# Performance work log

Hardware: AMD Instinct MI355X
Metric: run time of the kernel (lower is better)

The kernel has to match this reference:

```python
import jax, jax.numpy as jnp
import numpy as np

C_MID = 32  # inChannels // 8
# Packing order matches torch loop: diagonal offset -i for i in 0..C-1,
# i.e. pairs (j+i, j) for j in 0..C-1-i, concatenated.
_ROWS = np.concatenate([np.arange(C_MID - i) + i for i in range(C_MID)])
_COLS = np.concatenate([np.arange(C_MID - i) for i in range(C_MID)])


def _bn_relu(y, g, b, m, v, eps=1e-5):
    # y: (B, C, H, W); per-channel affine BN (eval-style) + relu
    inv = g / jnp.sqrt(v + eps)
    return jax.nn.relu(y * inv[:, None, None] + (b - m * inv)[:, None, None])


def setup_inputs() -> dict:
    key = jax.random.key(0)
    ks = jax.random.split(key, 14)
    B, Cin, H, W = 16, 256, 64, 64
    mid, T, Cout = C_MID, C_MID * (C_MID + 1) // 2, 256
    return {
        "x": jax.random.normal(ks[0], (B, Cin, H, W), jnp.float32),
        "w1": jax.random.normal(ks[1], (mid, Cin), jnp.float32) * 0.05,
        "b1": jax.random.normal(ks[2], (mid,), jnp.float32) * 0.05,
        "g1": jax.random.uniform(ks[3], (mid,), jnp.float32, 0.5, 1.5),
        "be1": jax.random.normal(ks[4], (mid,), jnp.float32) * 0.1,
        "m1": jax.random.normal(ks[5], (mid,), jnp.float32) * 0.1,
        "v1": jax.random.uniform(ks[6], (mid,), jnp.float32, 0.5, 1.5),
        "w2": jax.random.normal(ks[7], (Cout, T), jnp.float32) * 0.05,
        "b2": jax.random.normal(ks[8], (Cout,), jnp.float32) * 0.05,
        "g2": jax.random.uniform(ks[9], (Cout,), jnp.float32, 0.5, 1.5),
        "be2": jax.random.normal(ks[10], (Cout,), jnp.float32) * 0.1,
        "m2": jax.random.normal(ks[11], (Cout,), jnp.float32) * 0.1,
        "v2": jax.random.uniform(ks[12], (Cout,), jnp.float32, 0.5, 1.5),
    }


def reference(x, w1, b1, g1, be1, m1, v1, w2, b2, g2, be2, m2, v2):
    # dimReduceLayer1: 1x1 conv + BN + relu
    y = jnp.einsum('bchw,oc->bohw', x, w1) + b1[:, None, None]
    y = _bn_relu(y, g1, be1, m1, v1)                       # (B, mid, H, W)
    yb = jnp.transpose(y, (0, 2, 3, 1))                    # (B, H, W, mid)
    rows = jnp.asarray(_ROWS)
    cols = jnp.asarray(_COLS)
    # Packed lower-triangular bilinear features, exactly the torch diagonal+cat order.
    packed = yb[..., rows] * yb[..., cols]                 # (B, H, W, T)
    # dimReduceLayer2: 1x1 conv + BN + relu
    z = jnp.einsum('bhwt,ot->bohw', packed, w2) + b2[:, None, None]
    return _bn_relu(z, g2, be2, m2, v2)
```

## Files before the change

kernel.cpp:

```cpp
#include <hip/hip_runtime.h>

#define EPS 1e-5f

typedef float f32x4 __attribute__((ext_vector_type(4)));
typedef short bf16x8 __attribute__((ext_vector_type(8)));

__device__ __forceinline__ unsigned short f2bf(float f) {
  unsigned int u = __builtin_bit_cast(unsigned int, f);
  u = (u + 0x7FFFu + ((u >> 16) & 1u)) >> 16;
  return (unsigned short)u;
}

__global__ __launch_bounds__(256) void k_prep(
    const float* __restrict__ w1, const float* __restrict__ b1,
    const float* __restrict__ g1, const float* __restrict__ be1,
    const float* __restrict__ m1, const float* __restrict__ v1,
    const float* __restrict__ w2, const float* __restrict__ b2,
    const float* __restrict__ g2, const float* __restrict__ be2,
    const float* __restrict__ m2, const float* __restrict__ v2,
    float* __restrict__ beta1, float* __restrict__ beta2,
    unsigned short* __restrict__ w1b, unsigned short* __restrict__ w2f)
{
  int t = blockIdx.x * 256 + threadIdx.x;
  if (t < 139264) {
    int j = t & 7, l = (t >> 3) & 63, g = t >> 9;
    int ct = g & 15, ks = g >> 4;
    int k = ks * 32 + (l >> 4) * 8 + j;
    int ch = ct * 16 + (l & 15);
    float val = 0.f;
    if (k < 528) {
      float s2 = g2[ch] * rsqrtf(v2[ch] + EPS);
      val = w2[ch * 528 + k] * s2;
    }
    w2f[t] = f2bf(val);
  }
  if (t < 8192) {
    int j = t & 7, l = (t >> 3) & 63, g = t >> 9;
    int ct = g & 1, ks = g >> 1;
    int c = ks * 32 + (l >> 4) * 8 + j;
    int m = ct * 16 + (l & 15);
    float s1 = g1[m] * rsqrtf(v1[m] + EPS);
    w1b[t] = f2bf(w1[m * 256 + c] * s1);
  }
  if (t < 32) {
    float s1 = g1[t] * rsqrtf(v1[t] + EPS);
    beta1[t] = (b1[t] - m1[t]) * s1 + be1[t];
  }
  if (t < 256) {
    float s2 = g2[t] * rsqrtf(v2[t] + EPS);
    beta2[t] = (b2[t] - m2[t]) * s2 + be2[t];
  }
}

template<int I>
__device__ __forceinline__ void do_diag(const float* __restrict__ y,
                                        unsigned short* __restrict__ pr)
{
  constexpr int L = 32 - I;
  constexpr int base = 32 * I - (I * (I - 1)) / 2;
  float p[L];
#pragma unroll
  for (int j = 0; j < L; ++j) p[j] = y[I + j] * y[j];
  constexpr int s = (base & 1) ? 1 : 0;
  if constexpr (s != 0) pr[base] = f2bf(p[0]);
#pragma unroll
  for (int j = s; j + 1 < L; j += 2)
    *(unsigned int*)&pr[base + j] =
        (unsigned int)f2bf(p[j]) | ((unsigned int)f2bf(p[j + 1]) << 16);
  if constexpr (((L - s) & 1) != 0) pr[base + L - 1] = f2bf(p[L - 1]);
}

template<int S>
__device__ __forceinline__ void do_set(const float* __restrict__ y,
                                       unsigned short* __restrict__ pr)
{
  do_diag<S>(y, pr);
  do_diag<31 - S>(y, pr);
  do_diag<S + 8>(y, pr);
  do_diag<23 - S>(y, pr);
}

__global__ __launch_bounds__(256, 4) void k_fused(
    const float* __restrict__ x, const unsigned short* __restrict__ w1b,
    const float* __restrict__ beta1, const unsigned short* __restrict__ w2f,
    const float* __restrict__ beta2, float* __restrict__ out)
{
  __shared__ __align__(16) unsigned short pk[32 * 548];
  __shared__ __align__(8) float yf[32 * 34];
  int tid = threadIdx.x;
  int wv = tid >> 6, lane = tid & 63;
  int l15 = lane & 15, l4 = lane >> 4;
  int g = blockIdx.x;
  int orig = ((g & 7) << 8) + (g >> 3);
  int pb = orig * 32;
  int b = pb >> 12, hw0 = pb & 4095;
  const float* xb = x + ((size_t)b << 20) + hw0;

  unsigned short* xt = pk;
  {
    int q = tid & 7;
    int cg = tid >> 3;
#pragma unroll
    for (int pass = 0; pass < 2; ++pass) {
      int c4 = cg + pass * 32;
      float4 v[4];
#pragma unroll
      for (int i = 0; i < 4; ++i)
        v[i] = *(const float4*)&xb[(size_t)(4 * c4 + i) * 4096 + 4 * q];
#pragma unroll
      for (int s = 0; s < 4; ++s) {
        float e0 = ((const float*)&v[0])[s];
        float e1 = ((const float*)&v[1])[s];
        float e2 = ((const float*)&v[2])[s];
        float e3 = ((const float*)&v[3])[s];
        unsigned int lo = (unsigned int)f2bf(e0) | ((unsigned int)f2bf(e1) << 16);
        unsigned int hi = (unsigned int)f2bf(e2) | ((unsigned int)f2bf(e3) << 16);
        *(uint2*)&xt[(4 * q + s) * 276 + 4 * c4] = make_uint2(lo, hi);
      }
    }
  }
  __syncthreads();

  {
    int pxt = wv & 1, mt = wv >> 1;
    int px = pxt * 16 + l15;
    f32x4 acc1 = (f32x4){0.f, 0.f, 0.f, 0.f};
    const uint4* w1b4 = (const uint4*)w1b;
#pragma unroll
    for (int ks = 0; ks < 8; ++ks) {
      union { uint4 q; bf16x8 v; } A, B;
      A.q = w1b4[(ks * 2 + mt) * 64 + lane];
      const unsigned short* s = &xt[px * 276 + ks * 32 + l4 * 8];
      uint2 lo = *(const uint2*)s;
      uint2 hi = *(const uint2*)(s + 4);
      B.q = make_uint4(lo.x, lo.y, hi.x, hi.y);
      acc1 = __builtin_amdgcn_mfma_f32_16x16x32_bf16(A.v, B.v, acc1, 0, 0, 0);
    }
    int m0 = mt * 16 + l4 * 4;
#pragma unroll
    for (int r = 0; r < 4; ++r)
      yf[px * 34 + m0 + r] = fmaxf(acc1[r] + beta1[m0 + r], 0.f);
  }
  __syncthreads();

  {
    int px2 = tid & 31, set = tid >> 5;
    const float* yr = &yf[px2 * 34];
    unsigned short* pr = &pk[px2 * 548];
    float y[32];
#pragma unroll
    for (int k = 0; k < 16; ++k) {
      float2 v = *(const float2*)&yr[2 * k];
      y[2 * k] = v.x; y[2 * k + 1] = v.y;
    }
    switch (set) {
      case 0: do_set<0>(y, pr); break;
      case 1: do_set<1>(y, pr); break;
      case 2: do_set<2>(y, pr); break;
      case 3: do_set<3>(y, pr); break;
      case 4: do_set<4>(y, pr); break;
      case 5: do_set<5>(y, pr); break;
      case 6: do_set<6>(y, pr); break;
      default: do_set<7>(y, pr); break;
    }
    if (set < 4) {
      *(unsigned int*)&pr[528 + set * 4] = 0u;
      *(unsigned int*)&pr[530 + set * 4] = 0u;
    }
  }

  float bet[4][4];
#pragma unroll
  for (int ctl = 0; ctl < 4; ++ctl)
#pragma unroll
    for (int r = 0; r < 4; ++r)
      bet[ctl][r] = beta2[(wv * 4 + ctl) * 16 + l4 * 4 + r];

  __syncthreads();

  f32x4 acc[2][4];
#pragma unroll
  for (int a = 0; a < 2; ++a)
#pragma unroll
    for (int c = 0; c < 4; ++c)
      acc[a][c] = (f32x4){0.f, 0.f, 0.f, 0.f};

  const uint4* w2f4 = (const uint4*)w2f;
#pragma unroll
  for (int ks = 0; ks < 17; ++ks) {
    union { uint4 q; bf16x8 v; } A[4], B[2];
#pragma unroll
    for (int ctl = 0; ctl < 4; ++ctl)
      A[ctl].q = w2f4[(ks * 16 + wv * 4 + ctl) * 64 + lane];
#pragma unroll
    for (int pt = 0; pt < 2; ++pt) {
      const unsigned short* src = &pk[(pt * 16 + l15) * 548 + ks * 32 + l4 * 8];
      uint2 lo = *(const uint2*)src;
      uint2 hi = *(const uint2*)(src + 4);
      B[pt].q = make_uint4(lo.x, lo.y, hi.x, hi.y);
    }
#pragma unroll
    for (int pt = 0; pt < 2; ++pt)
#pragma unroll
      for (int ctl = 0; ctl < 4; ++ctl)
        acc[pt][ctl] = __builtin_amdgcn_mfma_f32_16x16x32_bf16(
            A[ctl].v, B[pt].v, acc[pt][ctl], 0, 0, 0);
  }

#pragma unroll
  for (int pt = 0; pt < 2; ++pt) {
    int hw = hw0 + pt * 16 + l15;
#pragma unroll
    for (int ctl = 0; ctl < 4; ++ctl) {
      int ch = (wv * 4 + ctl) * 16 + l4 * 4;
#pragma unroll
      for (int r = 0; r < 4; ++r) {
        float v = fmaxf(acc[pt][ctl][r] + bet[ctl][r], 0.f);
        out[(((size_t)b * 256 + (ch + r)) << 12) + hw] = v;
      }
    }
  }
}

extern "C" void kernel_launch(void* const* d_in, const int* in_sizes, int n_in,
                              void* d_out, int out_size, void* d_ws, size_t ws_size,
                              hipStream_t stream)
{
  const float* x   = (const float*)d_in[0];
  const float* w1  = (const float*)d_in[1];
  const float* b1  = (const float*)d_in[2];
  const float* g1  = (const float*)d_in[3];
  const float* be1 = (const float*)d_in[4];
  const float* m1  = (const float*)d_in[5];
  const float* v1  = (const float*)d_in[6];
  const float* w2  = (const float*)d_in[7];
  const float* b2  = (const float*)d_in[8];
  const float* g2  = (const float*)d_in[9];
  const float* be2 = (const float*)d_in[10];
  const float* m2  = (const float*)d_in[11];
  const float* v2  = (const float*)d_in[12];

  char* ws = (char*)d_ws;
  float*          beta1 = (float*)(ws);
  float*          beta2 = (float*)(ws + 128);
  unsigned short* w1b   = (unsigned short*)(ws + 1152);
  unsigned short* w2f   = (unsigned short*)(ws + 17536);
  float* out = (float*)d_out;

  k_prep<<<dim3(544), dim3(256), 0, stream>>>(
      w1, b1, g1, be1, m1, v1, w2, b2, g2, be2, m2, v2, beta1, beta2, w1b, w2f);
  k_fused<<<dim3(2048), dim3(256), 0, stream>>>(x, w1b, beta1, w2f, beta2, out);
}
```

Measured before the change: 48.60 us.

## Split fused kernel into layer1 and layer2 kernels with larger pixel tiles

The single fused kernel becomes two kernels. The first computes the 1x1 conv with BN and ReLU and writes bf16 activations to a workspace. The second expands the bilinear features for 128 pixels per block of 512 threads and runs the second GEMM, so each weight fragment load is reused across more pixel tiles. The float-to-bf16 conversion also switches to the packed hardware instruction. This adds a global round trip for the intermediate activations, an extra launch, and a large shared buffer (about 140KB) that limits the second kernel to one block per CU.

```diff
diff --git a/kernel.cpp b/kernel.cpp
--- a/kernel.cpp
+++ b/kernel.cpp
@@ -9,6 +9,15 @@
   unsigned int u = __builtin_bit_cast(unsigned int, f);
   u = (u + 0x7FFFu + ((u >> 16) & 1u)) >> 16;
   return (unsigned short)u;
+}
+__device__ __forceinline__ float bf2f(unsigned short h) {
+  unsigned int u = ((unsigned int)h) << 16;
+  return __builtin_bit_cast(float, u);
+}
+__device__ __forceinline__ unsigned int cvt2(float a, float b) {
+  unsigned int r;
+  asm("v_cvt_pk_bf16_f32 %0, %1, %2" : "=v"(r) : "v"(a), "v"(b));
+  return r;
 }
 
 __global__ __launch_bounds__(256) void k_prep(
@@ -52,41 +61,11 @@
   }
 }
 
-template<int I>
-__device__ __forceinline__ void do_diag(const float* __restrict__ y,
-                                        unsigned short* __restrict__ pr)
-{
-  constexpr int L = 32 - I;
-  constexpr int base = 32 * I - (I * (I - 1)) / 2;
-  float p[L];
-#pragma unroll
-  for (int j = 0; j < L; ++j) p[j] = y[I + j] * y[j];
-  constexpr int s = (base & 1) ? 1 : 0;
-  if constexpr (s != 0) pr[base] = f2bf(p[0]);
-#pragma unroll
-  for (int j = s; j + 1 < L; j += 2)
-    *(unsigned int*)&pr[base + j] =
-        (unsigned int)f2bf(p[j]) | ((unsigned int)f2bf(p[j + 1]) << 16);
-  if constexpr (((L - s) & 1) != 0) pr[base + L - 1] = f2bf(p[L - 1]);
-}
-
-template<int S>
-__device__ __forceinline__ void do_set(const float* __restrict__ y,
-                                       unsigned short* __restrict__ pr)
-{
-  do_diag<S>(y, pr);
-  do_diag<31 - S>(y, pr);
-  do_diag<S + 8>(y, pr);
-  do_diag<23 - S>(y, pr);
-}
-
-__global__ __launch_bounds__(256, 4) void k_fused(
+__global__ __launch_bounds__(256) void k_l1(
     const float* __restrict__ x, const unsigned short* __restrict__ w1b,
-    const float* __restrict__ beta1, const unsigned short* __restrict__ w2f,
-    const float* __restrict__ beta2, float* __restrict__ out)
-{
-  __shared__ __align__(16) unsigned short pk[32 * 548];
-  __shared__ __align__(8) float yf[32 * 34];
+    const float* __restrict__ beta1, unsigned short* __restrict__ yws)
+{
+  __shared__ __align__(16) unsigned short xt[32 * 276];
   int tid = threadIdx.x;
   int wv = tid >> 6, lane = tid & 63;
   int l15 = lane & 15, l4 = lane >> 4;
@@ -96,7 +75,6 @@
   int b = pb >> 12, hw0 = pb & 4095;
   const float* xb = x + ((size_t)b << 20) + hw0;
 
-  unsigned short* xt = pk;
   {
     int q = tid & 7;
     int cg = tid >> 3;
@@ -109,13 +87,12 @@
         v[i] = *(const float4*)&xb[(size_t)(4 * c4 + i) * 4096 + 4 * q];
 #pragma unroll
       for (int s = 0; s < 4; ++s) {
-        float e0 = ((const float*)&v[0])[s];
-        float e1 = ((const float*)&v[1])[s];
-        float e2 = ((const float*)&v[2])[s];
-        float e3 = ((const float*)&v[3])[s];
-        unsigned int lo = (unsigned int)f2bf(e0) | ((unsigned int)f2bf(e1) << 16);
-        unsigned int hi = (unsigned int)f2bf(e2) | ((unsigned int)f2bf(e3) << 16);
-        *(uint2*)&xt[(4 * q + s) * 276 + 4 * c4] = make_uint2(lo, hi);
+        const float* e0 = (const float*)&v[0];
+        const float* e1 = (const float*)&v[1];
+        const float* e2 = (const float*)&v[2];
+        const float* e3 = (const float*)&v[3];
+        *(uint2*)&xt[(4 * q + s) * 276 + 4 * c4] =
+            make_uint2(cvt2(e0[s], e1[s]), cvt2(e2[s], e3[s]));
       }
     }
   }
@@ -137,85 +114,144 @@
       acc1 = __builtin_amdgcn_mfma_f32_16x16x32_bf16(A.v, B.v, acc1, 0, 0, 0);
     }
     int m0 = mt * 16 + l4 * 4;
+    float v0 = fmaxf(acc1[0] + beta1[m0 + 0], 0.f);
+    float v1 = fmaxf(acc1[1] + beta1[m0 + 1], 0.f);
+    float v2 = fmaxf(acc1[2] + beta1[m0 + 2], 0.f);
+    float v3 = fmaxf(acc1[3] + beta1[m0 + 3], 0.f);
+    *(uint2*)&yws[(size_t)(pb + px) * 32 + m0] =
+        make_uint2(cvt2(v0, v1), cvt2(v2, v3));
+  }
+}
+
+template<int I>
+__device__ __forceinline__ void do_diag(const float* __restrict__ y,
+                                        unsigned short* __restrict__ pr)
+{
+  constexpr int L = 32 - I;
+  constexpr int base = 32 * I - (I * (I - 1)) / 2;
+  float p[L];
+#pragma unroll
+  for (int j = 0; j < L; ++j) p[j] = y[I + j] * y[j];
+  constexpr int s = (base & 1) ? 1 : 0;
+  if constexpr (s != 0) pr[base] = f2bf(p[0]);
+#pragma unroll
+  for (int j = s; j + 1 < L; j += 2)
+    *(unsigned int*)&pr[base + j] = cvt2(p[j], p[j + 1]);
+  if constexpr (((L - s) & 1) != 0) pr[base + L - 1] = f2bf(p[L - 1]);
+}
+
+template<int S>
+__device__ __forceinline__ void do_set(const float* __restrict__ y,
+                                       unsigned short* __restrict__ pr)
+{
+  do_diag<S>(y, pr);
+  do_diag<31 - S>(y, pr);
+  do_diag<S + 8>(y, pr);
+  do_diag<23 - S>(y, pr);
+}
+
+__device__ __forceinline__ void p2_slice(const unsigned short* __restrict__ yws,
+                                         int pb, int px_base,
+                                         unsigned short* __restrict__ pk,
+                                         int tid256)
+{
+  int px2 = tid256 & 31, set = tid256 >> 5;
+  int pxl = px_base + px2;
+  const uint4* y4 = (const uint4*)(yws + (size_t)(pb + pxl) * 32);
+  float y[32];
+#pragma unroll
+  for (int qq = 0; qq < 4; ++qq) {
+    uint4 v = y4[qq];
+    unsigned int ua[4] = {v.x, v.y, v.z, v.w};
+#pragma unroll
+    for (int w = 0; w < 4; ++w) {
+      y[qq * 8 + 2 * w]     = bf2f((unsigned short)(ua[w] & 0xFFFFu));
+      y[qq * 8 + 2 * w + 1] = bf2f((unsigned short)(ua[w] >> 16));
+    }
+  }
+  unsigned short* pr = &pk[pxl * 548];
+  switch (set) {
+    case 0: do_set<0>(y, pr); break;
+    case 1: do_set<1>(y, pr); break;
+    case 2: do_set<2>(y, pr); break;
+    case 3: do_set<3>(y, pr); break;
+    case 4: do_set<4>(y, pr); break;
+    case 5: do_set<5>(y, pr); break;
+    case 6: do_set<6>(y, pr); break;
+    default: do_set<7>(y, pr); break;
+  }
+  if (set < 4) {
+    *(unsigned int*)&pr[528 + set * 4] = 0u;
+    *(unsigned int*)&pr[530 + set * 4] = 0u;
+  }
+}
+
+__global__ __launch_bounds__(512) void k_l2(
+    const unsigned short* __restrict__ yws, const unsigned short* __restrict__ w2f,
+    const float* __restrict__ beta2, float* __restrict__ out)
+{
+  __shared__ __align__(16) unsigned short pk[128 * 548];
+  int tid = threadIdx.x;
+  int wv = tid >> 6, lane = tid & 63;
+  int l15 = lane & 15, l4 = lane >> 4;
+  int g = blockIdx.x;
+  int orig = ((g & 7) << 6) + (g >> 3);
+  int pb = orig * 128;
+  int b = pb >> 12, hw0 = pb & 4095;
+
+  {
+    int half = tid >> 8;
+    int tid256 = tid & 255;
+    p2_slice(yws, pb, half * 32, pk, tid256);
+    p2_slice(yws, pb, (2 + half) * 32, pk, tid256);
+  }
+
+  float bet[2][4];
+#pragma unroll
+  for (int ci = 0; ci < 2; ++ci)
 #pragma unroll
     for (int r = 0; r < 4; ++r)
-      yf[px * 34 + m0 + r] = fmaxf(acc1[r] + beta1[m0 + r], 0.f);
-  }
+      bet[ci][r] = beta2[(wv * 2 + ci) * 16 + l4 * 4 + r];
+
   __syncthreads();
 
-  {
-    int px2 = tid & 31, set = tid >> 5;
-    const float* yr = &yf[px2 * 34];
-    unsigned short* pr = &pk[px2 * 548];
-    float y[32];
-#pragma unroll
-    for (int k = 0; k < 16; ++k) {
-      float2 v = *(const float2*)&yr[2 * k];
-      y[2 * k] = v.x; y[2 * k + 1] = v.y;
-    }
-    switch (set) {
-      case 0: do_set<0>(y, pr); break;
-      case 1: do_set<1>(y, pr); break;
-      case 2: do_set<2>(y, pr); break;
-      case 3: do_set<3>(y, pr); break;
-      case 4: do_set<4>(y, pr); break;
-      case 5: do_set<5>(y, pr); break;
-      case 6: do_set<6>(y, pr); break;
-      default: do_set<7>(y, pr); break;
-    }
-    if (set < 4) {
-      *(unsigned int*)&pr[528 + set * 4] = 0u;
-      *(unsigned int*)&pr[530 + set * 4] = 0u;
-    }
-  }
-
-  float bet[4][4];
-#pragma unroll
-  for (int ctl = 0; ctl < 4; ++ctl)
-#pragma unroll
-    for (int r = 0; r < 4; ++r)
-      bet[ctl][r] = beta2[(wv * 4 + ctl) * 16 + l4 * 4 + r];
-
-  __syncthreads();
-
-  f32x4 acc[2][4];
-#pragma unroll
-  for (int a = 0; a < 2; ++a)
-#pragma unroll
-    for (int c = 0; c < 4; ++c)
+  f32x4 acc[8][2];
+#pragma unroll
+  for (int a = 0; a < 8; ++a)
+#pragma unroll
+    for (int c = 0; c < 2; ++c)
       acc[a][c] = (f32x4){0.f, 0.f, 0.f, 0.f};
 
   const uint4* w2f4 = (const uint4*)w2f;
-#pragma unroll
   for (int ks = 0; ks < 17; ++ks) {
-    union { uint4 q; bf16x8 v; } A[4], B[2];
-#pragma unroll
-    for (int ctl = 0; ctl < 4; ++ctl)
-      A[ctl].q = w2f4[(ks * 16 + wv * 4 + ctl) * 64 + lane];
-#pragma unroll
-    for (int pt = 0; pt < 2; ++pt) {
+    union { uint4 q; bf16x8 v; } A[2], B[8];
+#pragma unroll
+    for (int ci = 0; ci < 2; ++ci)
+      A[ci].q = w2f4[(ks * 16 + wv * 2 + ci) * 64 + lane];
+#pragma unroll
+    for (int pt = 0; pt < 8; ++pt) {
       const unsigned short* src = &pk[(pt * 16 + l15) * 548 + ks * 32 + l4 * 8];
       uint2 lo = *(const uint2*)src;
       uint2 hi = *(const uint2*)(src + 4);
       B[pt].q = make_uint4(lo.x, lo.y, hi.x, hi.y);
     }
 #pragma unroll
-    for (int pt = 0; pt < 2; ++pt)
-#pragma unroll
-      for (int ctl = 0; ctl < 4; ++ctl)
-        acc[pt][ctl] = __builtin_amdgcn_mfma_f32_16x16x32_bf16(
-            A[ctl].v, B[pt].v, acc[pt][ctl], 0, 0, 0);
-  }
-
-#pragma unroll
-  for (int pt = 0; pt < 2; ++pt) {
+    for (int pt = 0; pt < 8; ++pt)
+#pragma unroll
+      for (int ci = 0; ci < 2; ++ci)
+        acc[pt][ci] = __builtin_amdgcn_mfma_f32_16x16x32_bf16(
+            A[ci].v, B[pt].v, acc[pt][ci], 0, 0, 0);
+  }
+
+#pragma unroll
+  for (int pt = 0; pt < 8; ++pt) {
     int hw = hw0 + pt * 16 + l15;
 #pragma unroll
-    for (int ctl = 0; ctl < 4; ++ctl) {
-      int ch = (wv * 4 + ctl) * 16 + l4 * 4;
+    for (int ci = 0; ci < 2; ++ci) {
+      int ch = (wv * 2 + ci) * 16 + l4 * 4;
 #pragma unroll
       for (int r = 0; r < 4; ++r) {
-        float v = fmaxf(acc[pt][ctl][r] + bet[ctl][r], 0.f);
+        float v = fmaxf(acc[pt][ci][r] + bet[ci][r], 0.f);
         out[(((size_t)b * 256 + (ch + r)) << 12) + hw] = v;
       }
     }
@@ -245,9 +281,11 @@
   float*          beta2 = (float*)(ws + 128);
   unsigned short* w1b   = (unsigned short*)(ws + 1152);
   unsigned short* w2f   = (unsigned short*)(ws + 17536);
+  unsigned short* yws   = (unsigned short*)(ws + 296064);
   float* out = (float*)d_out;
 
   k_prep<<<dim3(544), dim3(256), 0, stream>>>(
       w1, b1, g1, be1, m1, v1, w2, b2, g2, be2, m2, v2, beta1, beta2, w1b, w2f);
-  k_fused<<<dim3(2048), dim3(256), 0, stream>>>(x, w1b, beta1, w2f, beta2, out);
-}
+  k_l1<<<dim3(2048), dim3(256), 0, stream>>>(x, w1b, beta1, yws);
+  k_l2<<<dim3(512), dim3(512), 0, stream>>>(yws, w2f, beta2, out);
+}
```

New measurement: 51.30 us. +5.6%, slower.
